# Optimization experiments

Hardware: AMD Instinct MI355X
Metric: run time of the kernel (lower is better)

Reference implementation:

```python
import jax, jax.numpy as jnp
import numpy as np
from jax import lax

B, C, L = 8, 512, 4096
G, K = 4, 3
PAD = 1
EPS = 1e-5


def setup_inputs() -> dict:
    key = jax.random.key(0)
    ks = jax.random.split(key, 8)
    inp = {
        "input_feat": jax.random.normal(ks[0], (B, C, L), dtype=jnp.float32),
        "x": jax.random.normal(ks[1], (B, C, L), dtype=jnp.float32),
        # depthwise Conv1d(channels, channels, k=3, pad=1, groups=channels): weight (C,1,K)
        "conv_w": jax.random.normal(ks[2], (C, 1, K), dtype=jnp.float32) * (1.0 / np.sqrt(K)),
        "conv_b": jax.random.normal(ks[3], (C,), dtype=jnp.float32) * 0.02,
        # BatchNorm1d affine params (module maps 'LN' -> BatchNorm1d)
        "bn_gamma": jnp.ones((C,), dtype=jnp.float32),
        "bn_beta": jnp.zeros((C,), dtype=jnp.float32),
        # offset/weight generators: Linear(C -> G*K). Source inits to zero (degenerate);
        # use small random values so the deformable path is exercised.
        "off_w": jax.random.normal(ks[4], (G * K, C), dtype=jnp.float32) * 0.02,
        "off_b": jax.random.normal(ks[5], (G * K,), dtype=jnp.float32) * 0.02,
        "wgt_w": jax.random.normal(ks[6], (G * K, C), dtype=jnp.float32) * 0.02,
        "wgt_b": jax.random.normal(ks[7], (G * K,), dtype=jnp.float32) * 0.02,
    }
    return inp


def _forward(x, conv_w, conv_b, bn_gamma, bn_beta, off_w, off_b, wgt_w, wgt_b):
    Bx, Cx, Lx = x.shape
    gs = Cx // G  # group size along channel axis

    # --- spectral_conv: depthwise conv1d + BatchNorm (batch stats) + exact GELU ---
    y = lax.conv_general_dilated(
        x, conv_w, window_strides=(1,), padding=[(PAD, PAD)],
        dimension_numbers=("NCH", "OIH", "NCH"), feature_group_count=Cx,
    ) + conv_b[None, :, None]
    mean = jnp.mean(y, axis=(0, 2), keepdims=True)
    var = jnp.var(y, axis=(0, 2), keepdims=True)
    y = (y - mean) * lax.rsqrt(var + EPS) * bn_gamma[None, :, None] + bn_beta[None, :, None]
    y = jax.nn.gelu(y, approximate=False)  # torch nn.GELU default is exact erf

    feat = y.transpose(0, 2, 1)  # (B, L, C)
    offsets = (feat @ off_w.T + off_b).reshape(Bx, Lx, G, K)
    weights = jax.nn.softmax((feat @ wgt_w.T + wgt_b).reshape(Bx, Lx, G, K), axis=-1)

    # --- deformable spectral gather + bilinear interp + softmax blend ---
    xg = x.transpose(0, 2, 1).reshape(Bx, Lx, G, gs)  # (B, L, G, gs)
    base = jnp.arange(gs, dtype=x.dtype)
    # sample positions: (B, L, G, K, gs)
    idx = jnp.clip(base[None, None, None, None, :] + offsets[..., None], 0.0, gs - 1)
    fl = jnp.floor(idx)
    frac = idx - fl
    fli = jnp.clip(fl, 0, gs - 1).astype(jnp.int32)
    cei = jnp.clip(jnp.ceil(idx), 0, gs - 1).astype(jnp.int32)

    xe = jnp.broadcast_to(xg[:, :, :, None, :], idx.shape)  # (B, L, G, K, gs)
    x_floor = jnp.take_along_axis(xe, fli, axis=-1)
    x_ceil = jnp.take_along_axis(xe, cei, axis=-1)
    interp = x_floor * (1.0 - frac) + x_ceil * frac  # (B, L, G, K, gs)

    out = jnp.sum(interp * weights[..., None], axis=3)  # (B, L, G, gs)
    return out.reshape(Bx, Lx, Cx).transpose(0, 2, 1)  # (B, C, L)


def reference(input_feat, x, conv_w, conv_b, bn_gamma, bn_beta, off_w, off_b, wgt_w, wgt_b):
    # input_feat is accepted but unused, matching the source forward signature.
    return _forward(x, conv_w, conv_b, bn_gamma, bn_beta, off_w, off_b, wgt_w, wgt_b)
```

## Files before the change

### kernel.cpp

```cpp
#include <hip/hip_runtime.h>
#include <math.h>

#define BB 8
#define CC 512
#define LL 4096
#define GG 4
#define KK 3
#define EPSV 1e-5f

#define TL 8
#define XSP (CC + 4)
#define FTP (CC + 24)


__device__ __forceinline__ float gelu_tanh(float z) {
    float z2 = z * z;
    float a  = 1.5957691216f * fmaf(0.044715f * z2, z, z);
    return z * __builtin_amdgcn_rcpf(1.f + __expf(-a));
}

__device__ __forceinline__ ushort f32_to_bf16(float f) {
    uint u = __float_as_uint(f);
    return (ushort)((u + 0x7fffu + ((u >> 16) & 1u)) >> 16);
}

__global__ __launch_bounds__(256) void conv_stats_kernel(
    const float* __restrict__ x, const float* __restrict__ conv_w,
    const float* __restrict__ conv_b, float* __restrict__ ws)
{
    const int c = blockIdx.x;
    const int b = blockIdx.y;
    const int t = threadIdx.x;

    const float w0 = conv_w[c * 3 + 0];
    const float w1 = conv_w[c * 3 + 1];
    const float w2 = conv_w[c * 3 + 2];
    const float cb = conv_b[c];
    const float* xr = x + ((size_t)b * CC + c) * LL;

    float s = 0.f, ss = 0.f;
#pragma unroll
    for (int i = 0; i < 4; ++i) {
        const int l0 = 4 * (t + 256 * i);
        float4 q = *reinterpret_cast<const float4*>(xr + l0);
        float lf = (l0 == 0) ? 0.f : xr[l0 - 1];
        float rt = (l0 + 4 >= LL) ? 0.f : xr[l0 + 4];
        float y;
        y = fmaf(w0, lf,  fmaf(w1, q.x, fmaf(w2, q.y, cb))); s += y; ss = fmaf(y, y, ss);
        y = fmaf(w0, q.x, fmaf(w1, q.y, fmaf(w2, q.z, cb))); s += y; ss = fmaf(y, y, ss);
        y = fmaf(w0, q.y, fmaf(w1, q.z, fmaf(w2, q.w, cb))); s += y; ss = fmaf(y, y, ss);
        y = fmaf(w0, q.z, fmaf(w1, q.w, fmaf(w2, rt,  cb))); s += y; ss = fmaf(y, y, ss);
    }

#pragma unroll
    for (int d = 32; d > 0; d >>= 1) {
        s  += __shfl_down(s,  d, 64);
        ss += __shfl_down(ss, d, 64);
    }
    __shared__ float ls[4], lss[4];
    const int wid = t >> 6, lane = t & 63;
    if (lane == 0) { ls[wid] = s; lss[wid] = ss; }
    __syncthreads();
    if (t == 0) {
        ws[c * 8 + b]        = ls[0] + ls[1] + ls[2] + ls[3];
        ws[4096 + c * 8 + b] = lss[0] + lss[1] + lss[2] + lss[3];
    }
}

__global__ __launch_bounds__(512) void bn_finalize_kernel(
    const float* __restrict__ bn_gamma, const float* __restrict__ bn_beta,
    float* __restrict__ ws)
{
    const int c = threadIdx.x;
    float s = 0.f, ss = 0.f;
#pragma unroll
    for (int b = 0; b < 8; ++b) {
        s  += ws[c * 8 + b];
        ss += ws[4096 + c * 8 + b];
    }
    const float inv  = 1.f / (float)(BB * LL);
    const float mean = s * inv;
    const float var  = ss * inv - mean * mean;
    const float sc   = bn_gamma[c] * rsqrtf(var + EPSV);
    ws[8192 + c] = sc;
    ws[8704 + c] = bn_beta[c] - mean * sc;
}

__global__ __launch_bounds__(256) void fused_kernel(
    const float* __restrict__ x,
    const float* __restrict__ conv_w, const float* __restrict__ conv_b,
    const float* __restrict__ off_w,  const float* __restrict__ off_b,
    const float* __restrict__ wgt_w,  const float* __restrict__ wgt_b,
    const float* __restrict__ ws, float* __restrict__ out)
{
    __shared__ float  xs[TL + 2][XSP];
    __shared__ ushort ftb[TL][FTP];
    __shared__ float  pr[TL][24];

    const int t = threadIdx.x;
    const int b = blockIdx.y;
    const int ltile = ((blockIdx.x & 7) << 6) + (blockIdx.x >> 3);
    const int l0 = ltile * TL;

    const float* xb = x + (size_t)b * CC * LL;
    const float* wsScale = ws + 8192;
    const float* wsShift = ws + 8704;

#pragma unroll
    for (int r = 0; r < 2; ++r) {
        const int c = t + (r << 8);
        const float* xr = xb + (size_t)c * LL;
        float v[TL + 2];
        v[0] = (l0 == 0) ? 0.f : xr[l0 - 1];
#pragma unroll
        for (int i = 0; i < TL / 4; ++i) {
            float4 q = *reinterpret_cast<const float4*>(xr + l0 + i * 4);
            v[1 + i * 4 + 0] = q.x; v[1 + i * 4 + 1] = q.y;
            v[1 + i * 4 + 2] = q.z; v[1 + i * 4 + 3] = q.w;
        }
        v[TL + 1] = (l0 + TL >= LL) ? 0.f : xr[l0 + TL];

#pragma unroll
        for (int i = 0; i < TL + 2; ++i) xs[i][c] = v[i];

        const float w0 = conv_w[c * 3 + 0];
        const float w1 = conv_w[c * 3 + 1];
        const float w2 = conv_w[c * 3 + 2];
        const float sc = wsScale[c];
        const float sh = fmaf(conv_b[c], sc, wsShift[c]);
#pragma unroll
        for (int l = 0; l < TL; ++l) {
            float conv = fmaf(w0, v[l], fmaf(w1, v[l + 1], w2 * v[l + 2]));
            float z = fmaf(sc, conv, sh);
            ftb[l][c] = f32_to_bf16(gelu_tanh(z));
        }
    }
    __syncthreads();

    if (t < 24 * TL) {
        const int o = t >> 3;
        const int l = t & (TL - 1);
        const float* W = (o < 12) ? (off_w + o * CC) : (wgt_w + (o - 12) * CC);
        const uint4* fp = reinterpret_cast<const uint4*>(&ftb[l][0]);
        float a0 = 0.f, a1 = 0.f, a2 = 0.f, a3 = 0.f;
#pragma unroll 4
        for (int i = 0; i < CC / 8; ++i) {
            uint4 u = fp[i];
            float4 wa = *reinterpret_cast<const float4*>(W + 8 * i);
            float4 wb = *reinterpret_cast<const float4*>(W + 8 * i + 4);
            a0 = fmaf(__uint_as_float(u.x << 16),          wa.x, a0);
            a1 = fmaf(__uint_as_float(u.x & 0xffff0000u),  wa.y, a1);
            a2 = fmaf(__uint_as_float(u.y << 16),          wa.z, a2);
            a3 = fmaf(__uint_as_float(u.y & 0xffff0000u),  wa.w, a3);
            a0 = fmaf(__uint_as_float(u.z << 16),          wb.x, a0);
            a1 = fmaf(__uint_as_float(u.z & 0xffff0000u),  wb.y, a1);
            a2 = fmaf(__uint_as_float(u.w << 16),          wb.z, a2);
            a3 = fmaf(__uint_as_float(u.w & 0xffff0000u),  wb.w, a3);
        }
        float dv = (a0 + a1) + (a2 + a3);
        dv += (o < 12) ? off_b[o] : wgt_b[o - 12];
        pr[l][o] = dv;
    }
    __syncthreads();

    if (t < TL * GG) {
        const int l = t >> 2, g = t & 3;
        float a  = pr[l][12 + g * 3 + 0];
        float b2 = pr[l][12 + g * 3 + 1];
        float c2 = pr[l][12 + g * 3 + 2];
        float m = fmaxf(a, fmaxf(b2, c2));
        float ea = __expf(a - m), eb = __expf(b2 - m), ec = __expf(c2 - m);
        float inv = __builtin_amdgcn_rcpf(ea + eb + ec);
        pr[l][12 + g * 3 + 0] = ea * inv;
        pr[l][12 + g * 3 + 1] = eb * inv;
        pr[l][12 + g * 3 + 2] = ec * inv;
    }
    __syncthreads();

    float* ob = out + (size_t)b * CC * LL;
#pragma unroll
    for (int r = 0; r < 2; ++r) {
        const int c = t + (r << 8);
        const int g = c >> 7;
        const float j = (float)(c & 127);
        const int gbase = g << 7;
        float oacc[TL];
#pragma unroll
        for (int l = 0; l < TL; ++l) oacc[l] = 0.f;

#pragma unroll
        for (int l = 0; l < TL; ++l) {
            const float* xrow = &xs[l + 1][gbase];
#pragma unroll
            for (int k = 0; k < KK; ++k) {
                const float off = pr[l][g * 3 + k];
                const float w   = pr[l][12 + g * 3 + k];
                float idx = fminf(fmaxf(j + off, 0.f), 127.f);
                float fl  = floorf(idx);
                float fr  = idx - fl;
                int i0 = (int)fl;
                int i1 = i0 + 1; if (i1 > 127) i1 = 127;
                float xf = xrow[i0];
                float xc = xrow[i1];
                oacc[l] = fmaf(w, fmaf(fr, xc - xf, xf), oacc[l]);
            }
        }
        float* orow = ob + (size_t)c * LL + l0;
#pragma unroll
        for (int i = 0; i < TL / 4; ++i) {
            *reinterpret_cast<float4*>(orow + i * 4) =
                make_float4(oacc[i * 4 + 0], oacc[i * 4 + 1], oacc[i * 4 + 2], oacc[i * 4 + 3]);
        }
    }
}

extern "C" void kernel_launch(void* const* d_in, const int* in_sizes, int n_in,
                              void* d_out, int out_size, void* d_ws, size_t ws_size,
                              hipStream_t stream) {
    const float* x      = (const float*)d_in[1];
    const float* conv_w = (const float*)d_in[2];
    const float* conv_b = (const float*)d_in[3];
    const float* bn_g   = (const float*)d_in[4];
    const float* bn_b   = (const float*)d_in[5];
    const float* off_w  = (const float*)d_in[6];
    const float* off_b  = (const float*)d_in[7];
    const float* wgt_w  = (const float*)d_in[8];
    const float* wgt_b  = (const float*)d_in[9];
    float* out = (float*)d_out;
    float* ws  = (float*)d_ws;

    conv_stats_kernel<<<dim3(CC, BB), 256, 0, stream>>>(x, conv_w, conv_b, ws);
    bn_finalize_kernel<<<1, 512, 0, stream>>>(bn_g, bn_b, ws);
    fused_kernel<<<dim3(LL / TL, BB), 256, 0, stream>>>(
        x, conv_w, conv_b, off_w, off_b, wgt_w, wgt_b, ws, out);
}
```

Before: 235.2 us.

## Use MFMA for projection, bf16 x tile, larger L tile, precomputed interp coefficients

Replaces the scalar bf16 dot-product projection with 16x16x32 bf16 MFMA, using weights pre-converted to bf16 in the finalize kernel. It doubles the L tile to 16 with 512 threads per block, stores the x tile in LDS as bf16, and precomputes per-(l,g,k) floor indices and blended bilinear weights. conv_stats gets its halo values via lane shuffles. The aim is to cut ALU and LDS cost in the fused kernel. The bf16 x in the gather lowers output precision.

```diff
diff --git a/kernel.cpp b/kernel.cpp
--- a/kernel.cpp
+++ b/kernel.cpp
@@ -8,10 +8,15 @@
 #define KK 3
 #define EPSV 1e-5f
 
-#define TL 8
-#define XSP (CC + 4)
-#define FTP (CC + 24)
-
+#define TL 16
+#define NTILE (LL / TL)
+#define XSL 18
+#define FTP 520
+#define WB_F32OFF 9216
+
+
+typedef float  f32x4_t  __attribute__((ext_vector_type(4)));
+typedef __bf16 bf16x8_t __attribute__((ext_vector_type(8)));
 
 __device__ __forceinline__ float gelu_tanh(float z) {
     float z2 = z * z;
@@ -22,6 +27,11 @@
 __device__ __forceinline__ ushort f32_to_bf16(float f) {
     uint u = __float_as_uint(f);
     return (ushort)((u + 0x7fffu + ((u >> 16) & 1u)) >> 16);
+}
+
+__device__ __forceinline__ f32x4_t mfma_bf16(uint4 a, uint4 b, f32x4_t c) {
+    return __builtin_amdgcn_mfma_f32_16x16x32_bf16(
+        __builtin_bit_cast(bf16x8_t, a), __builtin_bit_cast(bf16x8_t, b), c, 0, 0, 0);
 }
 
 __global__ __launch_bounds__(256) void conv_stats_kernel(
@@ -43,8 +53,10 @@
     for (int i = 0; i < 4; ++i) {
         const int l0 = 4 * (t + 256 * i);
         float4 q = *reinterpret_cast<const float4*>(xr + l0);
-        float lf = (l0 == 0) ? 0.f : xr[l0 - 1];
-        float rt = (l0 + 4 >= LL) ? 0.f : xr[l0 + 4];
+        float lf = __shfl_up(q.w, 1);
+        if ((t & 63) == 0) lf = (l0 == 0) ? 0.f : xr[l0 - 1];
+        float rt = __shfl_down(q.x, 1);
+        if ((t & 63) == 63) rt = (l0 + 4 >= LL) ? 0.f : xr[l0 + 4];
         float y;
         y = fmaf(w0, lf,  fmaf(w1, q.x, fmaf(w2, q.y, cb))); s += y; ss = fmaf(y, y, ss);
         y = fmaf(w0, q.x, fmaf(w1, q.y, fmaf(w2, q.z, cb))); s += y; ss = fmaf(y, y, ss);
@@ -69,147 +81,167 @@
 
 __global__ __launch_bounds__(512) void bn_finalize_kernel(
     const float* __restrict__ bn_gamma, const float* __restrict__ bn_beta,
+    const float* __restrict__ off_w, const float* __restrict__ wgt_w,
     float* __restrict__ ws)
 {
-    const int c = threadIdx.x;
-    float s = 0.f, ss = 0.f;
-#pragma unroll
-    for (int b = 0; b < 8; ++b) {
-        s  += ws[c * 8 + b];
-        ss += ws[4096 + c * 8 + b];
-    }
-    const float inv  = 1.f / (float)(BB * LL);
-    const float mean = s * inv;
-    const float var  = ss * inv - mean * mean;
-    const float sc   = bn_gamma[c] * rsqrtf(var + EPSV);
-    ws[8192 + c] = sc;
-    ws[8704 + c] = bn_beta[c] - mean * sc;
-}
-
-__global__ __launch_bounds__(256) void fused_kernel(
+    const int t = threadIdx.x;
+    {
+        const int c = t;
+        float s = 0.f, ss = 0.f;
+#pragma unroll
+        for (int b = 0; b < 8; ++b) {
+            s  += ws[c * 8 + b];
+            ss += ws[4096 + c * 8 + b];
+        }
+        const float inv  = 1.f / (float)(BB * LL);
+        const float mean = s * inv;
+        const float var  = ss * inv - mean * mean;
+        const float sc   = bn_gamma[c] * rsqrtf(var + EPSV);
+        ws[8192 + c] = sc;
+        ws[8704 + c] = bn_beta[c] - mean * sc;
+    }
+    ushort* wb = reinterpret_cast<ushort*>(ws + WB_F32OFF);
+    const int o  = t >> 4;
+    const int k0 = (t & 15) * 32;
+    uint* dst = reinterpret_cast<uint*>(wb + o * CC + k0);
+    if (o < 24) {
+        const float* src = (o < 12) ? (off_w + o * CC + k0) : (wgt_w + (o - 12) * CC + k0);
+#pragma unroll 4
+        for (int j = 0; j < 16; ++j) {
+            float2 v = *reinterpret_cast<const float2*>(src + 2 * j);
+            dst[j] = (uint)f32_to_bf16(v.x) | ((uint)f32_to_bf16(v.y) << 16);
+        }
+    } else {
+#pragma unroll 4
+        for (int j = 0; j < 16; ++j) dst[j] = 0u;
+    }
+}
+
+__global__ __launch_bounds__(512, 8) void fused_kernel(
     const float* __restrict__ x,
     const float* __restrict__ conv_w, const float* __restrict__ conv_b,
-    const float* __restrict__ off_w,  const float* __restrict__ off_b,
-    const float* __restrict__ wgt_w,  const float* __restrict__ wgt_b,
+    const float* __restrict__ off_b,  const float* __restrict__ wgt_b,
     const float* __restrict__ ws, float* __restrict__ out)
 {
-    __shared__ float  xs[TL + 2][XSP];
+    __shared__ ushort xsb[CC][XSL];
     __shared__ ushort ftb[TL][FTP];
     __shared__ float  pr[TL][24];
-
-    const int t = threadIdx.x;
-    const int b = blockIdx.y;
-    const int ltile = ((blockIdx.x & 7) << 6) + (blockIdx.x >> 3);
+    __shared__ int    pdI[TL][GG][KK];
+    __shared__ float  pdA[TL][GG][KK];
+    __shared__ float  pdB[TL][GG][KK];
+
+    const int t  = threadIdx.x;
+    const int b  = blockIdx.y;
+    const int bx = blockIdx.x;
+    const int ltile = ((bx & 7) << 5) | (bx >> 3);
     const int l0 = ltile * TL;
 
-    const float* xb = x + (size_t)b * CC * LL;
-    const float* wsScale = ws + 8192;
-    const float* wsShift = ws + 8704;
-
-#pragma unroll
-    for (int r = 0; r < 2; ++r) {
-        const int c = t + (r << 8);
-        const float* xr = xb + (size_t)c * LL;
-        float v[TL + 2];
-        v[0] = (l0 == 0) ? 0.f : xr[l0 - 1];
+    {
+        const int c = t;
+        const float* xr = x + ((size_t)b * CC + c) * LL;
+        float q[TL + 2];
+        q[0] = (l0 == 0) ? 0.f : xr[l0 - 1];
 #pragma unroll
         for (int i = 0; i < TL / 4; ++i) {
-            float4 q = *reinterpret_cast<const float4*>(xr + l0 + i * 4);
-            v[1 + i * 4 + 0] = q.x; v[1 + i * 4 + 1] = q.y;
-            v[1 + i * 4 + 2] = q.z; v[1 + i * 4 + 3] = q.w;
-        }
-        v[TL + 1] = (l0 + TL >= LL) ? 0.f : xr[l0 + TL];
-
-#pragma unroll
-        for (int i = 0; i < TL + 2; ++i) xs[i][c] = v[i];
-
-        const float w0 = conv_w[c * 3 + 0];
-        const float w1 = conv_w[c * 3 + 1];
-        const float w2 = conv_w[c * 3 + 2];
-        const float sc = wsScale[c];
-        const float sh = fmaf(conv_b[c], sc, wsShift[c]);
+            float4 v = *reinterpret_cast<const float4*>(xr + l0 + 4 * i);
+            q[1 + 4*i] = v.x; q[2 + 4*i] = v.y; q[3 + 4*i] = v.z; q[4 + 4*i] = v.w;
+        }
+        q[TL + 1] = (l0 + TL >= LL) ? 0.f : xr[l0 + TL];
+
+        uint* xrow = reinterpret_cast<uint*>(&xsb[c][0]);
+#pragma unroll
+        for (int jj = 0; jj < (TL + 2) / 2; ++jj)
+            xrow[jj] = (uint)f32_to_bf16(q[2*jj]) | ((uint)f32_to_bf16(q[2*jj+1]) << 16);
+
+        const float w0 = conv_w[c*3+0], w1 = conv_w[c*3+1], w2 = conv_w[c*3+2];
+        const float sc = ws[8192 + c];
+        const float sh = fmaf(conv_b[c], sc, ws[8704 + c]);
 #pragma unroll
         for (int l = 0; l < TL; ++l) {
-            float conv = fmaf(w0, v[l], fmaf(w1, v[l + 1], w2 * v[l + 2]));
+            float conv = fmaf(w0, q[l], fmaf(w1, q[l+1], w2 * q[l+2]));
             float z = fmaf(sc, conv, sh);
             ftb[l][c] = f32_to_bf16(gelu_tanh(z));
         }
     }
     __syncthreads();
 
-    if (t < 24 * TL) {
-        const int o = t >> 3;
-        const int l = t & (TL - 1);
-        const float* W = (o < 12) ? (off_w + o * CC) : (wgt_w + (o - 12) * CC);
-        const uint4* fp = reinterpret_cast<const uint4*>(&ftb[l][0]);
-        float a0 = 0.f, a1 = 0.f, a2 = 0.f, a3 = 0.f;
-#pragma unroll 4
-        for (int i = 0; i < CC / 8; ++i) {
-            uint4 u = fp[i];
-            float4 wa = *reinterpret_cast<const float4*>(W + 8 * i);
-            float4 wb = *reinterpret_cast<const float4*>(W + 8 * i + 4);
-            a0 = fmaf(__uint_as_float(u.x << 16),          wa.x, a0);
-            a1 = fmaf(__uint_as_float(u.x & 0xffff0000u),  wa.y, a1);
-            a2 = fmaf(__uint_as_float(u.y << 16),          wa.z, a2);
-            a3 = fmaf(__uint_as_float(u.y & 0xffff0000u),  wa.w, a3);
-            a0 = fmaf(__uint_as_float(u.z << 16),          wb.x, a0);
-            a1 = fmaf(__uint_as_float(u.z & 0xffff0000u),  wb.y, a1);
-            a2 = fmaf(__uint_as_float(u.w << 16),          wb.z, a2);
-            a3 = fmaf(__uint_as_float(u.w & 0xffff0000u),  wb.w, a3);
-        }
-        float dv = (a0 + a1) + (a2 + a3);
-        dv += (o < 12) ? off_b[o] : wgt_b[o - 12];
-        pr[l][o] = dv;
+    const int wv = t >> 6, lane = t & 63;
+    if (wv < 2) {
+        const int n  = lane & 15;
+        const int kb = (lane >> 4) * 8;
+        const ushort* wrow = reinterpret_cast<const ushort*>(ws + WB_F32OFF) + (wv * 16 + n) * CC + kb;
+        const ushort* arow = &ftb[n][kb];
+        f32x4_t acc = {0.f, 0.f, 0.f, 0.f};
+#pragma unroll
+        for (int s = 0; s < CC / 32; ++s) {
+            uint4 av = *reinterpret_cast<const uint4*>(arow + 32 * s);
+            uint4 bv = *reinterpret_cast<const uint4*>(wrow + 32 * s);
+            acc = mfma_bf16(av, bv, acc);
+        }
+        const int o = wv * 16 + n;
+        if (o < 24) {
+            float bias = (o < 12) ? off_b[o] : wgt_b[o - 12];
+            const int rb = (lane >> 4) * 4;
+#pragma unroll
+            for (int i = 0; i < 4; ++i) pr[rb + i][o] = acc[i] + bias;
+        }
     }
     __syncthreads();
 
     if (t < TL * GG) {
         const int l = t >> 2, g = t & 3;
-        float a  = pr[l][12 + g * 3 + 0];
-        float b2 = pr[l][12 + g * 3 + 1];
-        float c2 = pr[l][12 + g * 3 + 2];
-        float m = fmaxf(a, fmaxf(b2, c2));
-        float ea = __expf(a - m), eb = __expf(b2 - m), ec = __expf(c2 - m);
-        float inv = __builtin_amdgcn_rcpf(ea + eb + ec);
-        pr[l][12 + g * 3 + 0] = ea * inv;
-        pr[l][12 + g * 3 + 1] = eb * inv;
-        pr[l][12 + g * 3 + 2] = ec * inv;
-    }
-    __syncthreads();
-
-    float* ob = out + (size_t)b * CC * LL;
-#pragma unroll
-    for (int r = 0; r < 2; ++r) {
-        const int c = t + (r << 8);
-        const int g = c >> 7;
-        const float j = (float)(c & 127);
-        const int gbase = g << 7;
-        float oacc[TL];
-#pragma unroll
-        for (int l = 0; l < TL; ++l) oacc[l] = 0.f;
-
-#pragma unroll
-        for (int l = 0; l < TL; ++l) {
-            const float* xrow = &xs[l + 1][gbase];
-#pragma unroll
-            for (int k = 0; k < KK; ++k) {
-                const float off = pr[l][g * 3 + k];
-                const float w   = pr[l][12 + g * 3 + k];
-                float idx = fminf(fmaxf(j + off, 0.f), 127.f);
-                float fl  = floorf(idx);
-                float fr  = idx - fl;
-                int i0 = (int)fl;
-                int i1 = i0 + 1; if (i1 > 127) i1 = 127;
-                float xf = xrow[i0];
-                float xc = xrow[i1];
-                oacc[l] = fmaf(w, fmaf(fr, xc - xf, xf), oacc[l]);
+        float s0 = pr[l][12 + g*3 + 0];
+        float s1 = pr[l][12 + g*3 + 1];
+        float s2 = pr[l][12 + g*3 + 2];
+        float m  = fmaxf(s0, fmaxf(s1, s2));
+        float e0 = __expf(s0 - m), e1 = __expf(s1 - m), e2 = __expf(s2 - m);
+        float inv = __builtin_amdgcn_rcpf(e0 + e1 + e2);
+        float wk0 = e0 * inv, wk1 = e1 * inv, wk2 = e2 * inv;
+        float wks[3] = {wk0, wk1, wk2};
+#pragma unroll
+        for (int k = 0; k < KK; ++k) {
+            float off = pr[l][g*3 + k];
+            float fo  = floorf(off);
+            float fr  = off - fo;
+            pdI[l][g][k] = (int)fo;
+            pdA[l][g][k] = wks[k] * (1.f - fr);
+            pdB[l][g][k] = wks[k] * fr;
+        }
+    }
+    __syncthreads();
+
+    {
+        const int c  = t;
+        const int g  = c >> 7;
+        const int j  = c & 127;
+        const int gb = g << 7;
+        float* orow = out + ((size_t)b * CC + c) * LL + l0;
+#pragma unroll
+        for (int h = 0; h < 2; ++h) {
+            float acc[8];
+#pragma unroll
+            for (int l = 0; l < 8; ++l) acc[l] = 0.f;
+#pragma unroll
+            for (int l = 0; l < 8; ++l) {
+                const int ll = h * 8 + l;
+#pragma unroll
+                for (int k = 0; k < KK; ++k) {
+                    const int   fo = pdI[ll][g][k];
+                    const float wa = pdA[ll][g][k];
+                    const float wc = pdB[ll][g][k];
+                    int p  = j + fo;
+                    int i0 = min(max(p, 0), 127);
+                    int i1 = min(max(p + 1, 0), 127);
+                    float xf = __uint_as_float((uint)xsb[gb + i0][ll + 1] << 16);
+                    float xc = __uint_as_float((uint)xsb[gb + i1][ll + 1] << 16);
+                    acc[l] = fmaf(wa, xf, fmaf(wc, xc, acc[l]));
+                }
             }
-        }
-        float* orow = ob + (size_t)c * LL + l0;
-#pragma unroll
-        for (int i = 0; i < TL / 4; ++i) {
-            *reinterpret_cast<float4*>(orow + i * 4) =
-                make_float4(oacc[i * 4 + 0], oacc[i * 4 + 1], oacc[i * 4 + 2], oacc[i * 4 + 3]);
+#pragma unroll
+            for (int i = 0; i < 2; ++i) {
+                *reinterpret_cast<float4*>(orow + h * 8 + 4 * i) =
+                    make_float4(acc[4*i], acc[4*i+1], acc[4*i+2], acc[4*i+3]);
+            }
         }
     }
 }
@@ -230,7 +262,7 @@
     float* ws  = (float*)d_ws;
 
     conv_stats_kernel<<<dim3(CC, BB), 256, 0, stream>>>(x, conv_w, conv_b, ws);
-    bn_finalize_kernel<<<1, 512, 0, stream>>>(bn_g, bn_b, ws);
-    fused_kernel<<<dim3(LL / TL, BB), 256, 0, stream>>>(
-        x, conv_w, conv_b, off_w, off_b, wgt_w, wgt_b, ws, out);
-}
+    bn_finalize_kernel<<<1, 512, 0, stream>>>(bn_g, bn_b, off_w, wgt_w, ws);
+    fused_kernel<<<dim3(NTILE, BB), 512, 0, stream>>>(
+        x, conv_w, conv_b, off_b, wgt_b, ws, out);
+}
```

New measurement: 233.3 us. No clear change (-0.8%).
